# Kernel tuning notes

Measured on AMD Instinct MI355X. Metric: run time of the kernel, lower is better.

## Reference

```python
import jax, jax.numpy as jnp
import numpy as np

IMG_SIZE = 28
DEPTH = 1024
BATCH = 64


def setup_inputs() -> dict:
    key = jax.random.key(0)
    inputs = jax.random.normal(key, (BATCH, IMG_SIZE, IMG_SIZE, DEPTH), dtype=jnp.float32)
    return {"inputs": inputs}


def reference(inputs) -> jnp.ndarray:
    # inputs: [B, H, W, C] feature maps (H == W == img_size)
    B, H, W, C = inputs.shape
    n = H
    tau = 0.5 / (n * n)
    beta = 4.0

    # Per-(batch, channel) argmax over the flattened spatial map.
    # Row-major flatten matches tf.reshape(feature_map, [-1, 1]) + tf.argmax.
    flat = inputs.reshape(B, H * W, C)              # [B, HW, C]
    mu = jnp.argmax(flat, axis=1)                   # [B, C] int
    i_max = (mu // n)[:, None, None, :]             # [B, 1, 1, C]
    j_max = (mu % n)[:, None, None, :]              # [B, 1, 1, C]

    ii = jnp.arange(n)[None, :, None, None]         # [1, H, 1, 1]
    jj = jnp.arange(n)[None, None, :, None]         # [1, 1, W, 1]

    # L1 distance from the per-channel peak, triangular mask clipped at -1.
    dist = jnp.abs(ii - i_max) + jnp.abs(jj - j_max)          # [B, H, W, C]
    mask = tau * jnp.maximum(1.0 - beta * dist.astype(inputs.dtype) / n, -1.0)

    return inputs * mask
```

## Files before the change

kernel.cpp:

```cpp
#include <hip/hip_runtime.h>

constexpr int BN  = 64;
constexpr int HH  = 28;
constexpr int WW  = 28;
constexpr int CC  = 1024;
constexpr int HWP = HH * WW;
constexpr int CQ  = CC / 4;
constexpr float TAU = 0.5f / 784.0f;

constexpr int SPL = 112;
constexpr int KN  = 7;

typedef float f32x4 __attribute__((ext_vector_type(4)));

__device__ __forceinline__ int iabs(int x) { return x < 0 ? -x : x; }

__global__ __launch_bounds__(896, 7) void fused_mask_kernel(
    const f32x4* __restrict__ in4, f32x4* __restrict__ out4) {
  __shared__ float s_pv[SPL][32];
  __shared__ int   s_pi[SPL][32];
  __shared__ float s2v[14][32];
  __shared__ int   s2i[14][32];
  __shared__ int   s_peak[32];

  const int t  = threadIdx.x;
  const int q  = t & 7;
  const int s3 = t >> 3;
  const int b  = blockIdx.x >> 5;
  const int cg = blockIdx.x & 31;

  const size_t base = ((size_t)b * HWP + s3) * CQ + cg * 8 + q;
  const f32x4* src = in4 + base;
  f32x4*       dst = out4 + base;
  constexpr size_t KSTR = (size_t)SPL * CQ;

  f32x4 vv0 = src[0 * KSTR];
  f32x4 vv1 = src[1 * KSTR];
  f32x4 vv2 = src[2 * KSTR];
  f32x4 vv3 = src[3 * KSTR];
  f32x4 vv4 = src[4 * KSTR];
  f32x4 vv5 = src[5 * KSTR];
  f32x4 vv6 = src[6 * KSTR];
  asm volatile("" : "+v"(vv0), "+v"(vv1), "+v"(vv2), "+v"(vv3),
                    "+v"(vv4), "+v"(vv5), "+v"(vv6));

  float bm0 = -__builtin_inff(), bm1 = bm0, bm2 = bm0, bm3 = bm0;
  int   bi0 = s3, bi1 = s3, bi2 = s3, bi3 = s3;
#define AMAXK(k) { const int p = s3 + SPL * (k); \
    if (vv##k.x > bm0) { bm0 = vv##k.x; bi0 = p; } \
    if (vv##k.y > bm1) { bm1 = vv##k.y; bi1 = p; } \
    if (vv##k.z > bm2) { bm2 = vv##k.z; bi2 = p; } \
    if (vv##k.w > bm3) { bm3 = vv##k.w; bi3 = p; } }
  AMAXK(0) AMAXK(1) AMAXK(2) AMAXK(3) AMAXK(4) AMAXK(5) AMAXK(6)
#undef AMAXK

  const int c0 = q * 4;
  s_pv[s3][c0 + 0] = bm0; s_pi[s3][c0 + 0] = bi0;
  s_pv[s3][c0 + 1] = bm1; s_pi[s3][c0 + 1] = bi1;
  s_pv[s3][c0 + 2] = bm2; s_pi[s3][c0 + 2] = bi2;
  s_pv[s3][c0 + 3] = bm3; s_pi[s3][c0 + 3] = bi3;
  __syncthreads();

  if (t < 448) {
    const int c = t & 31, g = t >> 5;
    float bv = s_pv[g * 8][c];
    int   bx = s_pi[g * 8][c];
    #pragma unroll
    for (int u = 1; u < 8; ++u) {
      const float v = s_pv[g * 8 + u][c];
      const int   x = s_pi[g * 8 + u][c];
      if (v > bv || (v == bv && x < bx)) { bv = v; bx = x; }
    }
    s2v[g][c] = bv; s2i[g][c] = bx;
  }
  __syncthreads();
  if (t < 32) {
    float bv = s2v[0][t];
    int   bx = s2i[0][t];
    #pragma unroll
    for (int g = 1; g < 14; ++g) {
      const float v = s2v[g][t];
      const int   x = s2i[g][t];
      if (v > bv || (v == bv && x < bx)) { bv = v; bx = x; }
    }
    const int im = bx / 28;
    s_peak[t] = (im << 8) | (bx - im * 28);
  }
  __syncthreads();

  const int pk0 = s_peak[c0 + 0], pk1 = s_peak[c0 + 1];
  const int pk2 = s_peak[c0 + 2], pk3 = s_peak[c0 + 3];
  const int i0 = s3 / 28;
  const int j0 = s3 - i0 * 28;
  const int im0 = pk0 >> 8, im1 = pk1 >> 8, im2 = pk2 >> 8, im3 = pk3 >> 8;
  const int dj0 = iabs(j0 - (pk0 & 255));
  const int dj1 = iabs(j0 - (pk1 & 255));
  const int dj2 = iabs(j0 - (pk2 & 255));
  const int dj3 = iabs(j0 - (pk3 & 255));
  constexpr float MS = -(TAU / 7.0f);

#define APPLYK(k) { const int i = i0 + 4 * (k); f32x4 o; \
    o.x = vv##k.x * fmaxf(fmaf((float)(iabs(i - im0) + dj0), MS, TAU), -TAU); \
    o.y = vv##k.y * fmaxf(fmaf((float)(iabs(i - im1) + dj1), MS, TAU), -TAU); \
    o.z = vv##k.z * fmaxf(fmaf((float)(iabs(i - im2) + dj2), MS, TAU), -TAU); \
    o.w = vv##k.w * fmaxf(fmaf((float)(iabs(i - im3) + dj3), MS, TAU), -TAU); \
    __builtin_nontemporal_store(o, dst + (size_t)(k) * KSTR); }
  APPLYK(0) APPLYK(1) APPLYK(2) APPLYK(3) APPLYK(4) APPLYK(5) APPLYK(6)
#undef APPLYK
}

extern "C" void kernel_launch(void* const* d_in, const int* in_sizes, int n_in,
                              void* d_out, int out_size, void* d_ws, size_t ws_size,
                              hipStream_t stream) {
  const f32x4* in4  = (const f32x4*)d_in[0];
  f32x4*       out4 = (f32x4*)d_out;
  fused_mask_kernel<<<BN * 32, 896, 0, stream>>>(in4, out4);
}
```

Measured before the change: 76.66 us.

## Persistent 512-thread blocks with software-pipelined channel tiles and shuffle argmax

Each block now handles 4 consecutive 32-channel groups for one batch in sequence, using 512 threads that each hold 12-13 spatial positions. The next tile's first 8 vectors are prefetched while the current tile is reduced and written. The first reduction level now uses wave shuffles instead of a large shared-memory table. This aims to hide load latency and cut sync and LDS cost, but it uses many more registers and launches far fewer blocks (512), which may lower occupancy and memory parallelism.

```diff
diff --git a/kernel.cpp b/kernel.cpp
--- a/kernel.cpp
+++ b/kernel.cpp
@@ -8,105 +8,139 @@
 constexpr int CQ  = CC / 4;
 constexpr float TAU = 0.5f / 784.0f;
 
-constexpr int SPL = 112;
-constexpr int KN  = 7;
-
 typedef float f32x4 __attribute__((ext_vector_type(4)));
 
 __device__ __forceinline__ int iabs(int x) { return x < 0 ? -x : x; }
 
-__global__ __launch_bounds__(896, 7) void fused_mask_kernel(
+__global__ __launch_bounds__(512, 4) void fused_mask_kernel(
     const f32x4* __restrict__ in4, f32x4* __restrict__ out4) {
-  __shared__ float s_pv[SPL][32];
-  __shared__ int   s_pi[SPL][32];
-  __shared__ float s2v[14][32];
-  __shared__ int   s2i[14][32];
+  __shared__ float s2v[8][32];
+  __shared__ int   s2i[8][32];
   __shared__ int   s_peak[32];
 
   const int t  = threadIdx.x;
   const int q  = t & 7;
   const int s3 = t >> 3;
-  const int b  = blockIdx.x >> 5;
-  const int cg = blockIdx.x & 31;
+  const int bk = blockIdx.x;
+  const int b  = bk >> 3;
+  const int cg0 = (bk & 7) * 4;
 
-  const size_t base = ((size_t)b * HWP + s3) * CQ + cg * 8 + q;
-  const f32x4* src = in4 + base;
-  f32x4*       dst = out4 + base;
-  constexpr size_t KSTR = (size_t)SPL * CQ;
+  constexpr size_t KSTR = (size_t)64 * CQ;
 
-  f32x4 vv0 = src[0 * KSTR];
-  f32x4 vv1 = src[1 * KSTR];
-  f32x4 vv2 = src[2 * KSTR];
-  f32x4 vv3 = src[3 * KSTR];
-  f32x4 vv4 = src[4 * KSTR];
-  f32x4 vv5 = src[5 * KSTR];
-  f32x4 vv6 = src[6 * KSTR];
-  asm volatile("" : "+v"(vv0), "+v"(vv1), "+v"(vv2), "+v"(vv3),
-                    "+v"(vv4), "+v"(vv5), "+v"(vv6));
+  const f32x4* sp = in4  + ((size_t)b * HWP + s3) * CQ + cg0 * 8 + q;
+  f32x4*       dp = out4 + ((size_t)b * HWP + s3) * CQ + cg0 * 8 + q;
 
-  float bm0 = -__builtin_inff(), bm1 = bm0, bm2 = bm0, bm3 = bm0;
-  int   bi0 = s3, bi1 = s3, bi2 = s3, bi3 = s3;
-#define AMAXK(k) { const int p = s3 + SPL * (k); \
-    if (vv##k.x > bm0) { bm0 = vv##k.x; bi0 = p; } \
-    if (vv##k.y > bm1) { bm1 = vv##k.y; bi1 = p; } \
-    if (vv##k.z > bm2) { bm2 = vv##k.z; bi2 = p; } \
-    if (vv##k.w > bm3) { bm3 = vv##k.w; bi3 = p; } }
-  AMAXK(0) AMAXK(1) AMAXK(2) AMAXK(3) AMAXK(4) AMAXK(5) AMAXK(6)
-#undef AMAXK
-
-  const int c0 = q * 4;
-  s_pv[s3][c0 + 0] = bm0; s_pi[s3][c0 + 0] = bi0;
-  s_pv[s3][c0 + 1] = bm1; s_pi[s3][c0 + 1] = bi1;
-  s_pv[s3][c0 + 2] = bm2; s_pi[s3][c0 + 2] = bi2;
-  s_pv[s3][c0 + 3] = bm3; s_pi[s3][c0 + 3] = bi3;
-  __syncthreads();
-
-  if (t < 448) {
-    const int c = t & 31, g = t >> 5;
-    float bv = s_pv[g * 8][c];
-    int   bx = s_pi[g * 8][c];
-    #pragma unroll
-    for (int u = 1; u < 8; ++u) {
-      const float v = s_pv[g * 8 + u][c];
-      const int   x = s_pi[g * 8 + u][c];
-      if (v > bv || (v == bv && x < bx)) { bv = v; bx = x; }
-    }
-    s2v[g][c] = bv; s2i[g][c] = bx;
-  }
-  __syncthreads();
-  if (t < 32) {
-    float bv = s2v[0][t];
-    int   bx = s2i[0][t];
-    #pragma unroll
-    for (int g = 1; g < 14; ++g) {
-      const float v = s2v[g][t];
-      const int   x = s2i[g][t];
-      if (v > bv || (v == bv && x < bx)) { bv = v; bx = x; }
-    }
-    const int im = bx / 28;
-    s_peak[t] = (im << 8) | (bx - im * 28);
-  }
-  __syncthreads();
-
-  const int pk0 = s_peak[c0 + 0], pk1 = s_peak[c0 + 1];
-  const int pk2 = s_peak[c0 + 2], pk3 = s_peak[c0 + 3];
-  const int i0 = s3 / 28;
-  const int j0 = s3 - i0 * 28;
-  const int im0 = pk0 >> 8, im1 = pk1 >> 8, im2 = pk2 >> 8, im3 = pk3 >> 8;
-  const int dj0 = iabs(j0 - (pk0 & 255));
-  const int dj1 = iabs(j0 - (pk1 & 255));
-  const int dj2 = iabs(j0 - (pk2 & 255));
-  const int dj3 = iabs(j0 - (pk3 & 255));
+  const bool tail = (s3 < 16);
+  const int  i0 = s3 / 28;
+  const int  j0 = s3 - 28 * i0;
+  const int  c0 = q * 4;
   constexpr float MS = -(TAU / 7.0f);
 
-#define APPLYK(k) { const int i = i0 + 4 * (k); f32x4 o; \
-    o.x = vv##k.x * fmaxf(fmaf((float)(iabs(i - im0) + dj0), MS, TAU), -TAU); \
-    o.y = vv##k.y * fmaxf(fmaf((float)(iabs(i - im1) + dj1), MS, TAU), -TAU); \
-    o.z = vv##k.z * fmaxf(fmaf((float)(iabs(i - im2) + dj2), MS, TAU), -TAU); \
-    o.w = vv##k.w * fmaxf(fmaf((float)(iabs(i - im3) + dj3), MS, TAU), -TAU); \
-    __builtin_nontemporal_store(o, dst + (size_t)(k) * KSTR); }
-  APPLYK(0) APPLYK(1) APPLYK(2) APPLYK(3) APPLYK(4) APPLYK(5) APPLYK(6)
-#undef APPLYK
+  f32x4 A0, A1, A2, A3, A4, A5, A6, A7;
+  f32x4 B0, B1, B2, B3, B4, B5, B6, B7;
+  f32x4 X8, X9, X10, X11;
+  f32x4 XT = {0.0f, 0.0f, 0.0f, 0.0f};
+
+  A0 = sp[0 * KSTR]; A1 = sp[1 * KSTR]; A2 = sp[2 * KSTR]; A3 = sp[3 * KSTR];
+  A4 = sp[4 * KSTR]; A5 = sp[5 * KSTR]; A6 = sp[6 * KSTR]; A7 = sp[7 * KSTR];
+
+#define AM(v, k) { const int p = s3 + 64 * (k); \
+    if (v.x > bm0) { bm0 = v.x; bi0 = p; } \
+    if (v.y > bm1) { bm1 = v.y; bi1 = p; } \
+    if (v.z > bm2) { bm2 = v.z; bi2 = p; } \
+    if (v.w > bm3) { bm3 = v.w; bi3 = p; } }
+
+#define RED(bv, bx) { \
+    _Pragma("unroll") \
+    for (int st = 8; st < 64; st <<= 1) { \
+      const float ov = __shfl_xor(bv, st, 64); \
+      const int   ox = __shfl_xor(bx, st, 64); \
+      if (ov > bv || (ov == bv && ox < bx)) { bv = ov; bx = ox; } \
+    } }
+
+#define APK(v, off) { f32x4 o; \
+    o.x = v.x * fmaxf(fmaf((float)(iabs(i - im0) + iabs(j - jm0)), MS, TAU), -TAU); \
+    o.y = v.y * fmaxf(fmaf((float)(iabs(i - im1) + iabs(j - jm1)), MS, TAU), -TAU); \
+    o.z = v.z * fmaxf(fmaf((float)(iabs(i - im2) + iabs(j - jm2)), MS, TAU), -TAU); \
+    o.w = v.w * fmaxf(fmaf((float)(iabs(i - im3) + iabs(j - jm3)), MS, TAU), -TAU); \
+    __builtin_nontemporal_store(o, dp + (off)); \
+    j += 8; i += 2; if (j >= 28) { j -= 28; ++i; } }
+
+#define TILE(CUR, NXT, PF) { \
+     \
+     \
+    X8  = sp[ 8 * KSTR]; X9  = sp[ 9 * KSTR]; \
+    X10 = sp[10 * KSTR]; X11 = sp[11 * KSTR]; \
+    if (tail) XT = sp[12 * KSTR]; \
+    float bm0 = -__builtin_inff(), bm1 = bm0, bm2 = bm0, bm3 = bm0; \
+    int   bi0 = s3, bi1 = s3, bi2 = s3, bi3 = s3; \
+    AM(CUR##0, 0) AM(CUR##1, 1) AM(CUR##2, 2) AM(CUR##3, 3) \
+    AM(CUR##4, 4) AM(CUR##5, 5) AM(CUR##6, 6) AM(CUR##7, 7) \
+    AM(X8, 8) AM(X9, 9) AM(X10, 10) AM(X11, 11) \
+    if (tail) { const int p = s3 + 768; \
+      if (XT.x > bm0) { bm0 = XT.x; bi0 = p; } \
+      if (XT.y > bm1) { bm1 = XT.y; bi1 = p; } \
+      if (XT.z > bm2) { bm2 = XT.z; bi2 = p; } \
+      if (XT.w > bm3) { bm3 = XT.w; bi3 = p; } } \
+     \
+     \
+    asm volatile("" : "+v"(CUR##0), "+v"(CUR##1), "+v"(CUR##2), "+v"(CUR##3), \
+                      "+v"(CUR##4), "+v"(CUR##5), "+v"(CUR##6), "+v"(CUR##7), \
+                      "+v"(X8), "+v"(X9), "+v"(X10), "+v"(X11)); \
+     \
+     \
+    if (PF) { \
+      NXT##0 = sp[8 + 0 * KSTR]; NXT##1 = sp[8 + 1 * KSTR]; \
+      NXT##2 = sp[8 + 2 * KSTR]; NXT##3 = sp[8 + 3 * KSTR]; \
+      NXT##4 = sp[8 + 4 * KSTR]; NXT##5 = sp[8 + 5 * KSTR]; \
+      NXT##6 = sp[8 + 6 * KSTR]; NXT##7 = sp[8 + 7 * KSTR]; \
+    } \
+     \
+    RED(bm0, bi0) RED(bm1, bi1) RED(bm2, bi2) RED(bm3, bi3) \
+    if ((t & 56) == 0) { const int w = t >> 6; \
+      s2v[w][c0 + 0] = bm0; s2i[w][c0 + 0] = bi0; \
+      s2v[w][c0 + 1] = bm1; s2i[w][c0 + 1] = bi1; \
+      s2v[w][c0 + 2] = bm2; s2i[w][c0 + 2] = bi2; \
+      s2v[w][c0 + 3] = bm3; s2i[w][c0 + 3] = bi3; } \
+    __syncthreads(); \
+    if (t < 32) { \
+      float bv = s2v[0][t]; int bx = s2i[0][t]; \
+      _Pragma("unroll") \
+      for (int g = 1; g < 8; ++g) { \
+        const float v = s2v[g][t]; const int x = s2i[g][t]; \
+        if (v > bv || (v == bv && x < bx)) { bv = v; bx = x; } } \
+      const int im = bx / 28; \
+      s_peak[t] = (im << 8) | (bx - 28 * im); } \
+    __syncthreads(); \
+     \
+    { const int pk0 = s_peak[c0 + 0], pk1 = s_peak[c0 + 1]; \
+      const int pk2 = s_peak[c0 + 2], pk3 = s_peak[c0 + 3]; \
+      const int im0 = pk0 >> 8, jm0 = pk0 & 255; \
+      const int im1 = pk1 >> 8, jm1 = pk1 & 255; \
+      const int im2 = pk2 >> 8, jm2 = pk2 & 255; \
+      const int im3 = pk3 >> 8, jm3 = pk3 & 255; \
+      int i = i0, j = j0; \
+      APK(CUR##0, 0 * KSTR) APK(CUR##1, 1 * KSTR) APK(CUR##2, 2 * KSTR) \
+      APK(CUR##3, 3 * KSTR) APK(CUR##4, 4 * KSTR) APK(CUR##5, 5 * KSTR) \
+      APK(CUR##6, 6 * KSTR) APK(CUR##7, 7 * KSTR) \
+      APK(X8, 8 * KSTR) APK(X9, 9 * KSTR) APK(X10, 10 * KSTR) APK(X11, 11 * KSTR) \
+      if (tail) { f32x4 o; \
+        o.x = XT.x * fmaxf(fmaf((float)(iabs(i - im0) + iabs(j - jm0)), MS, TAU), -TAU); \
+        o.y = XT.y * fmaxf(fmaf((float)(iabs(i - im1) + iabs(j - jm1)), MS, TAU), -TAU); \
+        o.z = XT.z * fmaxf(fmaf((float)(iabs(i - im2) + iabs(j - jm2)), MS, TAU), -TAU); \
+        o.w = XT.w * fmaxf(fmaf((float)(iabs(i - im3) + iabs(j - jm3)), MS, TAU), -TAU); \
+        __builtin_nontemporal_store(o, dp + 12 * KSTR); } \
+    } }
+
+  TILE(A, B, true)  sp += 8; dp += 8;
+  TILE(B, A, true)  sp += 8; dp += 8;
+  TILE(A, B, true)  sp += 8; dp += 8;
+  TILE(B, A, false)
+
+#undef TILE
+#undef APK
+#undef RED
+#undef AM
 }
 
 extern "C" void kernel_launch(void* const* d_in, const int* in_sizes, int n_in,
@@ -114,5 +148,5 @@
                               hipStream_t stream) {
   const f32x4* in4  = (const f32x4*)d_in[0];
   f32x4*       out4 = (f32x4*)d_out;
-  fused_mask_kernel<<<BN * 32, 896, 0, stream>>>(in4, out4);
+  fused_mask_kernel<<<512, 512, 0, stream>>>(in4, out4);
 }
```

New measurement: 72.81 us. 5.0% less time.
